# Optimization experiments

Hardware: AMD Instinct MI355X
Metric: run time of the kernel (lower is better)

The kernel has to match this reference:

```python
import jax, jax.numpy as jnp
import numpy as np

GAMMA_LOCAL = 2.5
ALPHA = 1.2
DELTA = 1.0
TAU = 0.3
LAMBDA_CONTRAST = 0.5
EPS = 1e-7


def _corners(b):
    # b: [..., 4] in xywh format; returns corners and w,h, each [..., 1] (keepdims, matching torch.chunk)
    x, y, w, h = b[..., 0:1], b[..., 1:2], b[..., 2:3], b[..., 3:4]
    return x - w / 2, x + w / 2, y - h / 2, y + h / 2, w, h


def bbox_iou(box1, box2, ciou=False):
    # Faithful port of ultralytics bbox_iou (xywh=True). Output keeps a trailing dim of 1.
    b1x1, b1x2, b1y1, b1y2, w1, h1 = _corners(box1)
    b2x1, b2x2, b2y1, b2y2, w2, h2 = _corners(box2)
    inter = jnp.clip(jnp.minimum(b1x2, b2x2) - jnp.maximum(b1x1, b2x1), 0, None) * \
            jnp.clip(jnp.minimum(b1y2, b2y2) - jnp.maximum(b1y1, b2y1), 0, None)
    union = w1 * h1 + w2 * h2 - inter + EPS
    iou = inter / union
    if ciou:
        cw = jnp.maximum(b1x2, b2x2) - jnp.minimum(b1x1, b2x1)  # enclosing box width
        ch = jnp.maximum(b1y2, b2y2) - jnp.minimum(b1y1, b2y1)  # enclosing box height
        c2 = cw ** 2 + ch ** 2 + EPS
        rho2 = ((b2x1 + b2x2 - b1x1 - b1x2) ** 2 + (b2y1 + b2y2 - b1y1 - b1y2) ** 2) / 4
        v = (4 / np.pi ** 2) * (jnp.arctan(w2 / h2) - jnp.arctan(w1 / h1)) ** 2
        alpha = jax.lax.stop_gradient(v / (v - iou + (1 + EPS)))  # torch computes alpha under no_grad
        iou = iou - (rho2 / c2 + v * alpha)
    return iou


def setup_inputs() -> dict:
    key = jax.random.key(0)
    k1, k2, k3, k4, k5 = jax.random.split(key, 5)
    N, D, P = 8192, 256, 100
    pred_boxes = jax.random.uniform(k1, (N, 4), dtype=jnp.float32)
    target_boxes = jax.random.uniform(k2, (N, 4), dtype=jnp.float32)
    embeddings = jax.random.normal(k3, (N, D), dtype=jnp.float32)
    density_map = jax.random.uniform(k4, (N,), dtype=jnp.float32)
    indices = jax.random.randint(k5, (P, 2), 0, N, dtype=jnp.int64 if jax.config.jax_enable_x64 else jnp.int32)
    return {"pred_boxes": pred_boxes, "target_boxes": target_boxes,
            "embeddings": embeddings, "density_map": density_map, "indices": indices}


def reference(pred_boxes, target_boxes, embeddings, density_map, indices):
    # Localization term
    ious = bbox_iou(pred_boxes, target_boxes, ciou=True)            # [N, 1]
    area_norm = target_boxes[..., 2] * target_boxes[..., 3]          # [N]
    saf_ciou = (1 - ious) ** GAMMA_LOCAL / (area_norm + 1e-7)        # [N,1]/[N] -> [N,N] broadcast (as in torch)
    density_weight = 1 + ALPHA * density_map[..., None]              # [N, 1]
    hardness_weight = jax.nn.sigmoid(5.0 * (0.5 - jax.lax.stop_gradient(ious)))  # [N, 1]
    loss_loc = (density_weight * hardness_weight * saf_ciou).mean()

    # Contrastive term: vectorized version of the per-pair Python loop
    bi = pred_boxes[indices[:, 0]]                                   # [P, 4]
    bj = pred_boxes[indices[:, 1]]                                   # [P, 4]
    pair_iou = bbox_iou(bi, bj, ciou=False)[..., 0]                  # [P]
    mask = pair_iou > TAU                                            # [P] bool
    emb_dist = jnp.linalg.norm(embeddings[indices[:, 0]] - embeddings[indices[:, 1]], axis=-1)  # [P]
    pair_loss = jax.nn.relu(DELTA - emb_dist) ** 2                   # [P]
    contrastive_loss = jnp.sum(jnp.where(mask, pair_loss, 0.0))

    P = indices.shape[0]
    loss_contrast = LAMBDA_CONTRAST * contrastive_loss / (P + 1e-7)
    return loss_loc + loss_contrast
```

## Files before the change

### kernel.cpp

```cpp
#include <hip/hip_runtime.h>
#include <hip/hip_bf16.h>
#include <math.h>


#define NBLK 64
#define NTHR 256

__device__ __forceinline__ float iou_plain(float4 b1, float4 b2) {
    float b1x1 = b1.x - 0.5f * b1.z, b1x2 = b1.x + 0.5f * b1.z;
    float b1y1 = b1.y - 0.5f * b1.w, b1y2 = b1.y + 0.5f * b1.w;
    float b2x1 = b2.x - 0.5f * b2.z, b2x2 = b2.x + 0.5f * b2.z;
    float b2y1 = b2.y - 0.5f * b2.w, b2y2 = b2.y + 0.5f * b2.w;
    float iw = fmaxf(fminf(b1x2, b2x2) - fmaxf(b1x1, b2x1), 0.0f);
    float ih = fmaxf(fminf(b1y2, b2y2) - fmaxf(b1y1, b2y1), 0.0f);
    float inter = iw * ih;
    float uni = b1.z * b1.w + b2.z * b2.w - inter + 1e-7f;
    return inter / uni;
}

__device__ __forceinline__ float iou_ciou(float4 b1, float4 b2) {
    float b1x1 = b1.x - 0.5f * b1.z, b1x2 = b1.x + 0.5f * b1.z;
    float b1y1 = b1.y - 0.5f * b1.w, b1y2 = b1.y + 0.5f * b1.w;
    float b2x1 = b2.x - 0.5f * b2.z, b2x2 = b2.x + 0.5f * b2.z;
    float b2y1 = b2.y - 0.5f * b2.w, b2y2 = b2.y + 0.5f * b2.w;
    float iw = fmaxf(fminf(b1x2, b2x2) - fmaxf(b1x1, b2x1), 0.0f);
    float ih = fmaxf(fminf(b1y2, b2y2) - fmaxf(b1y1, b2y1), 0.0f);
    float inter = iw * ih;
    float uni = b1.z * b1.w + b2.z * b2.w - inter + 1e-7f;
    float iou = inter / uni;
    float cw = fmaxf(b1x2, b2x2) - fminf(b1x1, b2x1);
    float ch = fmaxf(b1y2, b2y2) - fminf(b1y1, b2y1);
    float c2 = cw * cw + ch * ch + 1e-7f;
    float dx = b2.x - b1.x, dy = b2.y - b1.y;
    float rho2 = dx * dx + dy * dy;
    float dat = atanf(b2.z / b2.w) - atanf(b1.z / b1.w);
    const float four_over_pi2 = 0.40528473456935108578f;
    float v = four_over_pi2 * dat * dat;
    float alpha = v / (v - iou + (1.0f + 1e-7f));
    return iou - (rho2 / c2 + v * alpha);
}

__global__ __launch_bounds__(NTHR) void partials_kernel(
    const float4* __restrict__ pred, const float4* __restrict__ targ,
    const float* __restrict__ emb, const float* __restrict__ dens,
    const int* __restrict__ idx, float* __restrict__ ws, int N, int P) {
    int tid = threadIdx.x;
    int gtid = blockIdx.x * NTHR + tid;
    int lane = tid & 63;

    float sA = 0.0f, sB = 0.0f, sC = 0.0f;

    for (int i = gtid; i < N; i += NBLK * NTHR) {
        float4 pb = pred[i];
        float4 tb = targ[i];
        float iou = iou_ciou(pb, tb);
        float om = 1.0f - iou;
        float saf = om * om * sqrtf(om);
        float hw = 1.0f / (1.0f + expf(5.0f * iou - 2.5f));
        sA += (1.0f + 1.2f * dens[i]) * hw * saf;
        sB += 1.0f / (tb.z * tb.w + 1e-7f);
    }

    int wid = gtid >> 6;
    if (wid < P) {
        int i0 = idx[2 * wid];
        int i1 = idx[2 * wid + 1];
        const float4* e0 = (const float4*)(emb + (size_t)i0 * 256);
        const float4* e1 = (const float4*)(emb + (size_t)i1 * 256);
        float4 a = e0[lane];
        float4 b = e1[lane];
        float dx = a.x - b.x, dy = a.y - b.y, dz = a.z - b.z, dw = a.w - b.w;
        float d2 = dx * dx + dy * dy + dz * dz + dw * dw;
        #pragma unroll
        for (int o = 32; o > 0; o >>= 1) d2 += __shfl_xor(d2, o);
        if (lane == 0) {
            float dist = sqrtf(d2);
            float pl = fmaxf(1.0f - dist, 0.0f);
            pl = pl * pl;
            float piou = iou_plain(pred[i0], pred[i1]);
            if (piou > 0.3f) sC += pl;
        }
    }

    #pragma unroll
    for (int o = 32; o > 0; o >>= 1) {
        sA += __shfl_xor(sA, o);
        sB += __shfl_xor(sB, o);
        sC += __shfl_xor(sC, o);
    }
    __shared__ float lred[4][3];
    if (lane == 0) {
        int w = tid >> 6;
        lred[w][0] = sA; lred[w][1] = sB; lred[w][2] = sC;
    }
    __syncthreads();
    if (tid == 0) {
        float a = 0.0f, b = 0.0f, c = 0.0f;
        #pragma unroll
        for (int w = 0; w < 4; w++) { a += lred[w][0]; b += lred[w][1]; c += lred[w][2]; }
        ws[blockIdx.x] = a;
        ws[NBLK + blockIdx.x] = b;
        ws[2 * NBLK + blockIdx.x] = c;
    }
}

__global__ __launch_bounds__(64) void finalize_kernel(
    const float* __restrict__ ws, float* __restrict__ out, float n2, float pdenom) {
    int t = threadIdx.x;
    float a = ws[t];
    float b = ws[NBLK + t];
    float c = ws[2 * NBLK + t];
    #pragma unroll
    for (int o = 32; o > 0; o >>= 1) {
        a += __shfl_xor(a, o);
        b += __shfl_xor(b, o);
        c += __shfl_xor(c, o);
    }
    if (t == 0) {
        out[0] = (a * b) / n2 + 0.5f * c / pdenom;
    }
}

extern "C" void kernel_launch(void* const* d_in, const int* in_sizes, int n_in,
                              void* d_out, int out_size, void* d_ws, size_t ws_size,
                              hipStream_t stream) {
    const float4* pred = (const float4*)d_in[0];
    const float4* targ = (const float4*)d_in[1];
    const float* emb   = (const float*)d_in[2];
    const float* dens  = (const float*)d_in[3];
    const int* idx     = (const int*)d_in[4];
    float* out = (float*)d_out;
    float* ws  = (float*)d_ws;

    int N = in_sizes[0] / 4;
    int P = in_sizes[4] / 2;

    partials_kernel<<<NBLK, NTHR, 0, stream>>>(pred, targ, emb, dens, idx, ws, N, P);
    float n2 = (float)N * (float)N;
    float pdenom = (float)P + 1e-7f;
    finalize_kernel<<<1, 64, 0, stream>>>(ws, out, n2, pdenom);
}
```

Measured before the change: 67.20 us.

## Fuse partial and finalize kernels into a single-block kernel

```diff
diff --git a/kernel.cpp b/kernel.cpp
--- a/kernel.cpp
+++ b/kernel.cpp
@@ -3,8 +3,7 @@
 #include <math.h>
 
 
-#define NBLK 64
-#define NTHR 256
+#define NTHR 1024
 
 __device__ __forceinline__ float iou_plain(float4 b1, float4 b2) {
     float b1x1 = b1.x - 0.5f * b1.z, b1x2 = b1.x + 0.5f * b1.z;
@@ -40,35 +39,34 @@
     return iou - (rho2 / c2 + v * alpha);
 }
 
-__global__ __launch_bounds__(NTHR) void partials_kernel(
+__global__ __launch_bounds__(NTHR) void fused_kernel(
     const float4* __restrict__ pred, const float4* __restrict__ targ,
     const float* __restrict__ emb, const float* __restrict__ dens,
-    const int* __restrict__ idx, float* __restrict__ ws, int N, int P) {
+    const int* __restrict__ idx, float* __restrict__ out, int N, int P) {
     int tid = threadIdx.x;
-    int gtid = blockIdx.x * NTHR + tid;
     int lane = tid & 63;
+    int wid = tid >> 6;
 
     float sA = 0.0f, sB = 0.0f, sC = 0.0f;
 
-    for (int i = gtid; i < N; i += NBLK * NTHR) {
+    #pragma unroll 4
+    for (int i = tid; i < N; i += NTHR) {
         float4 pb = pred[i];
         float4 tb = targ[i];
+        float dn = dens[i];
         float iou = iou_ciou(pb, tb);
-        float om = 1.0f - iou;
+        float om = fmaxf(1.0f - iou, 0.0f);
         float saf = om * om * sqrtf(om);
         float hw = 1.0f / (1.0f + expf(5.0f * iou - 2.5f));
-        sA += (1.0f + 1.2f * dens[i]) * hw * saf;
+        sA += (1.0f + 1.2f * dn) * hw * saf;
         sB += 1.0f / (tb.z * tb.w + 1e-7f);
     }
 
-    int wid = gtid >> 6;
-    if (wid < P) {
-        int i0 = idx[2 * wid];
-        int i1 = idx[2 * wid + 1];
-        const float4* e0 = (const float4*)(emb + (size_t)i0 * 256);
-        const float4* e1 = (const float4*)(emb + (size_t)i1 * 256);
-        float4 a = e0[lane];
-        float4 b = e1[lane];
+    for (int p = wid; p < P; p += (NTHR / 64)) {
+        int i0 = idx[2 * p];
+        int i1 = idx[2 * p + 1];
+        float4 a = ((const float4*)(emb + (size_t)i0 * 256))[lane];
+        float4 b = ((const float4*)(emb + (size_t)i1 * 256))[lane];
         float dx = a.x - b.x, dy = a.y - b.y, dz = a.z - b.z, dw = a.w - b.w;
         float d2 = dx * dx + dy * dy + dz * dz + dw * dw;
         #pragma unroll
@@ -88,36 +86,19 @@
         sB += __shfl_xor(sB, o);
         sC += __shfl_xor(sC, o);
     }
-    __shared__ float lred[4][3];
+    __shared__ float red[NTHR / 64][3];
     if (lane == 0) {
-        int w = tid >> 6;
-        lred[w][0] = sA; lred[w][1] = sB; lred[w][2] = sC;
+        red[wid][0] = sA; red[wid][1] = sB; red[wid][2] = sC;
     }
     __syncthreads();
     if (tid == 0) {
         float a = 0.0f, b = 0.0f, c = 0.0f;
         #pragma unroll
-        for (int w = 0; w < 4; w++) { a += lred[w][0]; b += lred[w][1]; c += lred[w][2]; }
-        ws[blockIdx.x] = a;
-        ws[NBLK + blockIdx.x] = b;
-        ws[2 * NBLK + blockIdx.x] = c;
-    }
-}
-
-__global__ __launch_bounds__(64) void finalize_kernel(
-    const float* __restrict__ ws, float* __restrict__ out, float n2, float pdenom) {
-    int t = threadIdx.x;
-    float a = ws[t];
-    float b = ws[NBLK + t];
-    float c = ws[2 * NBLK + t];
-    #pragma unroll
-    for (int o = 32; o > 0; o >>= 1) {
-        a += __shfl_xor(a, o);
-        b += __shfl_xor(b, o);
-        c += __shfl_xor(c, o);
-    }
-    if (t == 0) {
-        out[0] = (a * b) / n2 + 0.5f * c / pdenom;
+        for (int w = 0; w < NTHR / 64; w++) {
+            a += red[w][0]; b += red[w][1]; c += red[w][2];
+        }
+        float n2 = (float)N * (float)N;
+        out[0] = (a * b) / n2 + 0.5f * c / ((float)P + 1e-7f);
     }
 }
 
@@ -130,13 +111,9 @@
     const float* dens  = (const float*)d_in[3];
     const int* idx     = (const int*)d_in[4];
     float* out = (float*)d_out;
-    float* ws  = (float*)d_ws;
 
     int N = in_sizes[0] / 4;
     int P = in_sizes[4] / 2;
 
-    partials_kernel<<<NBLK, NTHR, 0, stream>>>(pred, targ, emb, dens, idx, ws, N, P);
-    float n2 = (float)N * (float)N;
-    float pdenom = (float)P + 1e-7f;
-    finalize_kernel<<<1, 64, 0, stream>>>(ws, out, n2, pdenom);
+    fused_kernel<<<1, NTHR, 0, stream>>>(pred, targ, emb, dens, idx, out, N, P);
 }
```

Result: slower. 83.09 us (+23.7%).
